# Optimization experiments

Hardware: AMD Instinct MI355X
Metric: run time of the kernel (lower is better)

## Reference

```python
import jax, jax.numpy as jnp
import numpy as np

B, L, U, H = 16, 1024, 512, 2  # batch, seq_len, units, highway_num


def setup_inputs() -> dict:
    key = jax.random.key(0)
    ks = jax.random.split(key, 8)
    s = 0.02  # weight init scale
    return {
        "inputs": jax.random.normal(ks[0], (B, L, U), dtype=jnp.float32),
        "tW": jax.random.normal(ks[1], (H, U, U), dtype=jnp.float32) * s,
        "tb": jnp.zeros((H, U), dtype=jnp.float32),
        "cW": jax.random.normal(ks[2], (H, U, U), dtype=jnp.float32) * s,
        "cb": jnp.zeros((H, U), dtype=jnp.float32),
        "aW": jax.random.normal(ks[3], (3 * U,), dtype=jnp.float32) * s,
        "ab": jnp.zeros((1,), dtype=jnp.float32),
        "frW": jax.random.normal(ks[4], (2 * U, U), dtype=jnp.float32) * s,
        "frb": jnp.zeros((U,), dtype=jnp.float32),
        "ffW": jax.random.normal(ks[5], (2 * U, U), dtype=jnp.float32) * s,
        "ffb": jnp.zeros((U,), dtype=jnp.float32),
    }


def reference(inputs, tW, tb, cW, cb, aW, ab, frW, frb, ffW, ffb):
    # Highway stack (inference: dropout is identity)
    x = inputs
    for i in range(tW.shape[0]):
        t = jax.nn.relu(x @ tW[i] + tb[i])
        c = jax.nn.sigmoid(x @ cW[i] + cb[i])
        x = t * c + x * (1.0 - c)

    # Pairwise MLP self-attention.
    # Original: A_ij = relu(dense1(concat([x_i, x_j, x_i*x_j]))).
    # Split aW = [w1; w2; w3] so we never materialize the [B,L,L,3U] tensor:
    # A_ij = relu(x_i.w1 + x_j.w2 + sum_d x_i_d * x_j_d * w3_d + b)
    u = x.shape[-1]
    w1, w2, w3 = aW[:u], aW[u:2 * u], aW[2 * u:]
    s1 = x @ w1                                    # [B,L]
    s2 = x @ w2                                    # [B,L]
    s3 = jnp.einsum('bid,bjd->bij', x * w3, x)     # [B,L,L]
    A = jax.nn.relu(s1[:, :, None] + s2[:, None, :] + s3 + ab[0])
    att = jnp.einsum('bij,bjd->bid', jax.nn.softmax(A, axis=-1), x)

    # Fuse gate. NOTE: original code uses fuse_f_dense (sigmoid) for BOTH
    # z and f (fuse_z_dense is never called), so z == f at inference.
    concat = jnp.concatenate([inputs, att], axis=-1)  # [B,L,2U]
    z = jax.nn.sigmoid(concat @ ffW + ffb)
    r = jax.nn.sigmoid(concat @ frW + frb)
    f = z
    return r * inputs + f * z
```

## Files before the change

### kernel.cpp

```cpp
#include <hip/hip_runtime.h>
#include <math.h>

typedef __bf16 bf16;
typedef __attribute__((ext_vector_type(8))) __bf16 bf16x8;
typedef __attribute__((ext_vector_type(4))) float f32x4;

#define CDIV(a,b) (((a)+(b)-1)/(b))


__device__ __forceinline__ void load_lds16(const bf16* g, bf16* l) {
  __builtin_amdgcn_global_load_lds(
      (const __attribute__((address_space(1))) unsigned int*)(g),
      (__attribute__((address_space(3))) unsigned int*)(l), 16, 0, 0);
}

struct GemmArgs {
  const bf16* A; const bf16* B; bf16* C;
  int K, lda, ldb, ldc;
  long long Ab, Bb, Cb;
  const float* s1; const float* s2; const float* abp;
  float* lsum;
  int L;
  int gxsh, gysh;
};

template<int EPI>
__global__ __launch_bounds__(256, 4)
void gemm_nt(GemmArgs g) {
  __shared__ bf16 As[128 * 64];
  __shared__ bf16 Bs[128 * 64];
  const int tid = threadIdx.x;
  const int bid = blockIdx.x;
  const int xcd = bid & 7;
  const int t = bid >> 3;
  const int bx = t & ((1 << g.gxsh) - 1);
  const int r  = t >> g.gxsh;
  const int Rx = gridDim.x >> (3 + g.gxsh);
  const int gr = xcd * Rx + r;
  const int by = gr & ((1 << g.gysh) - 1);
  const int bz = gr >> g.gysh;

  const bf16* Ag = g.A + (long long)bz * g.Ab + (long long)(by * 128) * g.lda;
  const bf16* Bg = g.B + (long long)bz * g.Bb + (long long)(bx * 128) * g.ldb;
  const int wid = tid >> 6, lane = tid & 63;
  const int wm = (wid >> 1) << 6;
  const int wn = (wid & 1) << 6;
  const int lr = lane & 15, lq = lane >> 4;

  f32x4 acc[4][4];
#pragma unroll
  for (int i = 0; i < 4; i++)
#pragma unroll
    for (int j = 0; j < 4; j++) acc[i][j] = f32x4{0.f, 0.f, 0.f, 0.f};

  const int srow8 = (tid >> 3) & 7;
  const int skc   = (tid & 7) ^ srow8;
  const int lswz  = (lr & 7);

  for (int k0 = 0; k0 < g.K; k0 += 64) {
    __syncthreads();
#pragma unroll
    for (int j = 0; j < 4; j++) {
      const int ci = (tid >> 6) * 4 + j;
      const int row = ci * 8 + srow8;
      load_lds16(Ag + (long long)row * g.lda + k0 + skc * 8, As + ci * 512);
      load_lds16(Bg + (long long)row * g.ldb + k0 + skc * 8, Bs + ci * 512);
    }
    __syncthreads();
#pragma unroll
    for (int ks = 0; ks < 2; ks++) {
      bf16x8 af[4], bfr[4];
      const int kx = (ks * 4 + lq) ^ lswz;
#pragma unroll
      for (int i = 0; i < 4; i++)
        af[i] = *(const bf16x8*)(&As[(wm + i * 16 + lr) * 64 + kx * 8]);
#pragma unroll
      for (int j = 0; j < 4; j++)
        bfr[j] = *(const bf16x8*)(&Bs[(wn + j * 16 + lr) * 64 + kx * 8]);
#pragma unroll
      for (int i = 0; i < 4; i++)
#pragma unroll
        for (int j = 0; j < 4; j++)
          acc[i][j] = __builtin_amdgcn_mfma_f32_16x16x32_bf16(af[i], bfr[j], acc[i][j], 0, 0, 0);
    }
  }

  bf16* Cg = g.C + (long long)bz * g.Cb;
#pragma unroll
  for (int i = 0; i < 4; i++) {
#pragma unroll
    for (int v = 0; v < 4; v++) {
      int row = by * 128 + wm + i * 16 + lq * 4 + v;
      float srow = 0.f;
      if (EPI == 1) srow = g.s1[bz * g.L + row] + g.abp[0];
      if (EPI == 4) srow = 1.f / g.s1[bz * g.L + row];
      float psum = 0.f;
#pragma unroll
      for (int j = 0; j < 4; j++) {
        int col = bx * 128 + wn + j * 16 + lr;
        float val = acc[i][j][v];
        if (EPI == 1) {
          val += srow + g.s2[bz * g.L + col];
          val = fminf(fmaxf(val, 0.f), 60.f);
          val = __expf(val);
          bf16 eb = (bf16)val;
          psum += (float)eb;
          Cg[(long long)row * g.ldc + col] = eb;
        } else {
          val *= srow;
          Cg[(long long)row * g.ldc + col] = (bf16)val;
        }
      }
      if (EPI == 1) {
        psum += __shfl_xor(psum, 1, 64);
        psum += __shfl_xor(psum, 2, 64);
        psum += __shfl_xor(psum, 4, 64);
        psum += __shfl_xor(psum, 8, 64);
        if (lr == 0) atomicAdd(&g.lsum[bz * g.L + row], psum);
      }
    }
  }
}

struct DualArgs {
  const bf16* A; const bf16* A2;
  const bf16* Bt;
  void* C; const void* xres;
  const float* bias_t; const float* bias_c;
  int K, ldb;
  const float* aW;
  float* s1a; float* s2a;
  bf16* q;
};

template<int EPI>
__global__ __launch_bounds__(256, 4)
void gemm_dual(DualArgs g) {
  __shared__ bf16 As[128 * 64];
  __shared__ bf16 Bs[128 * 64];
  const int tid = threadIdx.x;
  const int bid = blockIdx.x;
  const int xcd = bid & 7;
  const int t = bid >> 3;
  const int bx = t & 7;
  const int r  = t >> 3;
  const int Rx = gridDim.x >> 6;
  const int by = xcd * Rx + r;

  const int wid = tid >> 6, lane = tid & 63;
  const int wm = (wid >> 1) << 6;
  const int wn = (wid & 1) << 6;
  const int lr = lane & 15, lq = lane >> 4;

  f32x4 acc[4][4];
#pragma unroll
  for (int i = 0; i < 4; i++)
#pragma unroll
    for (int j = 0; j < 4; j++) acc[i][j] = f32x4{0.f, 0.f, 0.f, 0.f};

  const int srow8 = (tid >> 3) & 7;
  const int skc   = (tid & 7) ^ srow8;
  const int lswz  = (lr & 7);
  const long long abase = (long long)(by * 128) * 512;

  for (int k0 = 0; k0 < g.K; k0 += 64) {
    const bf16* Ak = (k0 < 512) ? g.A : g.A2;
    const int kk = k0 & 511;
    __syncthreads();
#pragma unroll
    for (int j = 0; j < 4; j++) {
      const int ci = (tid >> 6) * 4 + j;
      const int bn = ci * 8 + srow8;
      load_lds16(Ak + abase + (long long)bn * 512 + kk + skc * 8, As + ci * 512);
      const int grp = bn >> 5, r5 = bn & 31;
      const int grow = ((grp & 1) << 9) + bx * 64 + ((grp >> 1) << 5) + r5;
      load_lds16(g.Bt + (long long)grow * g.ldb + k0 + skc * 8, Bs + ci * 512);
    }
    __syncthreads();
#pragma unroll
    for (int ks = 0; ks < 2; ks++) {
      bf16x8 af[4], bfr[4];
      const int kx = (ks * 4 + lq) ^ lswz;
#pragma unroll
      for (int i = 0; i < 4; i++)
        af[i] = *(const bf16x8*)(&As[(wm + i * 16 + lr) * 64 + kx * 8]);
#pragma unroll
      for (int j = 0; j < 4; j++)
        bfr[j] = *(const bf16x8*)(&Bs[(wn + j * 16 + lr) * 64 + kx * 8]);
#pragma unroll
      for (int i = 0; i < 4; i++)
#pragma unroll
        for (int j = 0; j < 4; j++)
          acc[i][j] = __builtin_amdgcn_mfma_f32_16x16x32_bf16(af[i], bfr[j], acc[i][j], 0, 0, 0);
    }
  }

  const int colb = bx * 64 + (wn >> 1);
#pragma unroll
  for (int i = 0; i < 4; i++) {
#pragma unroll
    for (int v = 0; v < 4; v++) {
      int row = by * 128 + wm + i * 16 + lq * 4 + v;
      float p1s = 0.f, p2s = 0.f;
#pragma unroll
      for (int j = 0; j < 2; j++) {
        int col = colb + j * 16 + lr;
        long long idx = (long long)row * 512 + col;
        float p0 = acc[i][j][v] + g.bias_t[col];
        float p1 = acc[i][j + 2][v] + g.bias_c[col];
        if (EPI == 1) {
          float z = 1.f / (1.f + __expf(-p0));
          float rr = 1.f / (1.f + __expf(-p1));
          float x = ((const float*)g.xres)[idx];
          ((float*)g.C)[idx] = rr * x + z * z;
        } else {
          float tt = fmaxf(p0, 0.f);
          float c = 1.f / (1.f + __expf(-p1));
          float x = (float)((const bf16*)g.xres)[idx];
          bf16 xn = (bf16)(tt * c + x * (1.f - c));
          ((bf16*)g.C)[idx] = xn;
          if (EPI == 2) {
            float xf = (float)xn;
            p1s += xf * g.aW[col];
            p2s += xf * g.aW[512 + col];
            g.q[idx] = (bf16)(xf * g.aW[1024 + col]);
          }
        }
      }
      if (EPI == 2) {
        p1s += __shfl_xor(p1s, 1, 64);
        p1s += __shfl_xor(p1s, 2, 64);
        p1s += __shfl_xor(p1s, 4, 64);
        p1s += __shfl_xor(p1s, 8, 64);
        p2s += __shfl_xor(p2s, 1, 64);
        p2s += __shfl_xor(p2s, 2, 64);
        p2s += __shfl_xor(p2s, 4, 64);
        p2s += __shfl_xor(p2s, 8, 64);
        if (lr == 0) {
          atomicAdd(&g.s1a[row], p1s);
          atomicAdd(&g.s2a[row], p2s);
        }
      }
    }
  }
}

__global__ void wprep(const float* tW, const float* tb, const float* cW, const float* cb,
                      const float* frW, const float* frb, const float* ffW, const float* ffb,
                      bf16* w1T, bf16* w2T, float* bias1, float* bias2) {
  int idx = blockIdx.x * 256 + threadIdx.x;
  const int N1 = 1048576, N2 = 1048576;
  if (idx < N1) {
    int l = idx >> 19;
    int rem = idx & 524287;
    int n = rem >> 9, k = rem & 511;
    float v = (n < 512) ? tW[l * 262144 + k * 512 + n]
                        : cW[l * 262144 + k * 512 + (n - 512)];
    w1T[idx] = (bf16)v;
  } else if (idx < N1 + N2) {
    int j = idx - N1;
    int n = j >> 10, k = j & 1023;
    float v = (n < 512) ? ffW[k * 512 + n] : frW[k * 512 + (n - 512)];
    w2T[j] = (bf16)v;
  } else if (idx < N1 + N2 + 3072) {
    int j = idx - (N1 + N2);
    if (j < 2048) {
      int l = j >> 10, n = j & 1023;
      bias1[j] = (n < 512) ? tb[l * 512 + n] : cb[l * 512 + (n - 512)];
    } else {
      int n = j - 2048;
      bias2[n] = (n < 512) ? ffb[n] : frb[n - 512];
    }
  }
}

__global__ void init_conv(const float* inp, bf16* xb0) {
  long long i8 = ((long long)blockIdx.x * 256 + threadIdx.x) * 8;
  bf16x8 o;
#pragma unroll
  for (int k = 0; k < 8; k++) o[k] = (bf16)inp[i8 + k];
  *(bf16x8*)(xb0 + i8) = o;
}

__global__ __launch_bounds__(256) void transpose_k(const bf16* xb, bf16* xT) {
  __shared__ bf16 t[64][65];
  int b = blockIdx.z;
  int d0 = blockIdx.x * 64, j0 = blockIdx.y * 64;
  const bf16* src = xb + (long long)b * 524288;
  bf16* dst = xT + (long long)b * 524288;
  int tid = threadIdx.x;
  int rr = tid >> 3, cc = (tid & 7) * 8;
#pragma unroll
  for (int it = 0; it < 2; ++it) {
    int r = rr + it * 32;
    bf16x8 v = *(const bf16x8*)(src + (long long)(j0 + r) * 512 + d0 + cc);
#pragma unroll
    for (int k = 0; k < 8; k++) t[cc + k][r] = v[k];
  }
  __syncthreads();
#pragma unroll
  for (int it = 0; it < 2; ++it) {
    int r = rr + it * 32;
    bf16x8 v;
#pragma unroll
    for (int k = 0; k < 8; k++) v[k] = t[r][cc + k];
    *(bf16x8*)(dst + (long long)(d0 + r) * 1024 + j0 + cc) = v;
  }
}

extern "C" void kernel_launch(void* const* d_in, const int* in_sizes, int n_in,
                              void* d_out, int out_size, void* d_ws, size_t ws_size,
                              hipStream_t stream) {
  const float* inp = (const float*)d_in[0];
  const float* tW  = (const float*)d_in[1];
  const float* tb  = (const float*)d_in[2];
  const float* cW  = (const float*)d_in[3];
  const float* cb  = (const float*)d_in[4];
  const float* aW  = (const float*)d_in[5];
  const float* ab  = (const float*)d_in[6];
  const float* frW = (const float*)d_in[7];
  const float* frb = (const float*)d_in[8];
  const float* ffW = (const float*)d_in[9];
  const float* ffb = (const float*)d_in[10];
  float* out = (float*)d_out;

  char* p = (char*)d_ws;
  auto alloc = [&](size_t bytes) { char* r = p; p += (bytes + 255) & ~size_t(255); return r; };
  bf16* xb0   = (bf16*) alloc(16777216);
  bf16* x1    = (bf16*) alloc(16777216);
  bf16* x2    = (bf16*) alloc(16777216);
  bf16* q16   = (bf16*) alloc(16777216);
  bf16* xT16  = (bf16*) alloc(16777216);
  bf16* att16 = (bf16*) alloc(16777216);
  bf16* E16   = (bf16*) alloc(33554432);
  float* sred = (float*)alloc(196608);
  bf16* w1T   = (bf16*) alloc(2097152);
  bf16* w2T   = (bf16*) alloc(2097152);
  float* bias1= (float*)alloc(8192);
  float* bias2= (float*)alloc(4096);
  float* s1 = sred, *s2 = sred + 16384, *lsum = sred + 32768;

  hipMemsetAsync(sred, 0, 196608, stream);
  wprep<<<CDIV(1048576 + 1048576 + 3072, 256), 256, 0, stream>>>(
      tW, tb, cW, cb, frW, frb, ffW, ffb, w1T, w2T, bias1, bias2);
  init_conv<<<4096, 256, 0, stream>>>(inp, xb0);

  {
    DualArgs g{};
    g.A = xb0; g.A2 = xb0; g.Bt = w1T;
    g.C = x1; g.xres = xb0;
    g.bias_t = bias1; g.bias_c = bias1 + 512;
    g.K = 512; g.ldb = 512;
    gemm_dual<0><<<1024, 256, 0, stream>>>(g);
  }
  {
    DualArgs g{};
    g.A = x1; g.A2 = x1; g.Bt = w1T + 524288;
    g.C = x2; g.xres = x1;
    g.bias_t = bias1 + 1024; g.bias_c = bias1 + 1536;
    g.K = 512; g.ldb = 512;
    g.aW = aW; g.s1a = s1; g.s2a = s2; g.q = q16;
    gemm_dual<2><<<1024, 256, 0, stream>>>(g);
  }

  transpose_k<<<dim3(8, 16, 16), 256, 0, stream>>>(x2, xT16);

  {
    GemmArgs g{};
    g.A = q16; g.B = x2; g.C = E16;
    g.K = 512; g.lda = 512; g.ldb = 512; g.ldc = 1024;
    g.Ab = 524288; g.Bb = 524288; g.Cb = 1048576;
    g.s1 = s1; g.s2 = s2; g.abp = ab; g.lsum = lsum; g.L = 1024;
    g.gxsh = 3; g.gysh = 3;
    gemm_nt<1><<<1024, 256, 0, stream>>>(g);
  }
  {
    GemmArgs g{};
    g.A = E16; g.B = xT16; g.C = att16;
    g.K = 1024; g.lda = 1024; g.ldb = 1024; g.ldc = 512;
    g.Ab = 1048576; g.Bb = 524288; g.Cb = 524288;
    g.s1 = lsum; g.L = 1024;
    g.gxsh = 2; g.gysh = 3;
    gemm_nt<4><<<512, 256, 0, stream>>>(g);
  }
  {
    DualArgs g{};
    g.A = xb0; g.A2 = att16; g.Bt = w2T;
    g.C = out; g.xres = inp;
    g.bias_t = bias2; g.bias_c = bias2 + 512;
    g.K = 1024; g.ldb = 1024;
    gemm_dual<1><<<1024, 256, 0, stream>>>(g);
  }
}
```

Measured before the change: 271.7 us.

## Fuse transpose into highway GEMM epilogue and merge prep kernels

```diff
diff --git a/kernel.cpp b/kernel.cpp
--- a/kernel.cpp
+++ b/kernel.cpp
@@ -131,13 +131,15 @@
   const float* aW;
   float* s1a; float* s2a;
   bf16* q;
+  bf16* xT;
 };
 
 template<int EPI>
 __global__ __launch_bounds__(256, 4)
 void gemm_dual(DualArgs g) {
-  __shared__ bf16 As[128 * 64];
-  __shared__ bf16 Bs[128 * 64];
+  __shared__ bf16 smem[2 * 128 * 64];
+  bf16* As = smem;
+  bf16* Bs = smem + 8192;
   const int tid = threadIdx.x;
   const int bid = blockIdx.x;
   const int xcd = bid & 7;
@@ -196,6 +198,7 @@
   }
 
   const int colb = bx * 64 + (wn >> 1);
+  bf16 xn_arr[4][4][2];
 #pragma unroll
   for (int i = 0; i < 4; i++) {
 #pragma unroll
@@ -220,6 +223,7 @@
           bf16 xn = (bf16)(tt * c + x * (1.f - c));
           ((bf16*)g.C)[idx] = xn;
           if (EPI == 2) {
+            xn_arr[i][v][j] = xn;
             float xf = (float)xn;
             p1s += xf * g.aW[col];
             p2s += xf * g.aW[512 + col];
@@ -243,27 +247,59 @@
       }
     }
   }
+
+  if (EPI == 2) {
+    bf16* Ts = smem;
+    __syncthreads();
+#pragma unroll
+    for (int i = 0; i < 4; i++)
+#pragma unroll
+      for (int v = 0; v < 4; v++)
+#pragma unroll
+        for (int j = 0; j < 2; j++) {
+          int rloc = wm + i * 16 + lq * 4 + v;
+          int cloc = (wn >> 1) + j * 16 + lr;
+          Ts[cloc * 136 + rloc] = xn_arr[i][v][j];
+        }
+    __syncthreads();
+    const int b = by >> 3;
+    bf16* dst = g.xT + (long long)b * 524288 + ((by & 7) * 128);
+#pragma unroll
+    for (int it = 0; it < 2; it++) {
+      int d = (tid >> 3) + it * 32;
+      int jb = (tid & 7) * 16;
+      bf16x8 v0 = *(const bf16x8*)(&Ts[d * 136 + jb]);
+      bf16x8 v1 = *(const bf16x8*)(&Ts[d * 136 + jb + 8]);
+      long long o = (long long)(bx * 64 + d) * 1024 + jb;
+      *(bf16x8*)(dst + o) = v0;
+      *(bf16x8*)(dst + o + 8) = v1;
+    }
+  }
 }
 
-__global__ void wprep(const float* tW, const float* tb, const float* cW, const float* cb,
-                      const float* frW, const float* frb, const float* ffW, const float* ffb,
-                      bf16* w1T, bf16* w2T, float* bias1, float* bias2) {
-  int idx = blockIdx.x * 256 + threadIdx.x;
-  const int N1 = 1048576, N2 = 1048576;
+__global__ void prep(const float* tW, const float* tb, const float* cW, const float* cb,
+                     const float* frW, const float* frb, const float* ffW, const float* ffb,
+                     const float* inp, bf16* xb0,
+                     bf16* w1T, bf16* w2T, float* bias1, float* bias2, float* sred) {
+  const long long idx = (long long)blockIdx.x * 256 + threadIdx.x;
+  const long long N1 = 1048576, N2 = 1048576;
+  const long long T0 = N1 + N2 + 3072;
+  const long long T1 = T0 + 1048576;
+  const long long T2 = T1 + 12288;
   if (idx < N1) {
-    int l = idx >> 19;
-    int rem = idx & 524287;
+    int l = (int)(idx >> 19);
+    int rem = (int)(idx & 524287);
     int n = rem >> 9, k = rem & 511;
     float v = (n < 512) ? tW[l * 262144 + k * 512 + n]
                         : cW[l * 262144 + k * 512 + (n - 512)];
     w1T[idx] = (bf16)v;
   } else if (idx < N1 + N2) {
-    int j = idx - N1;
+    int j = (int)(idx - N1);
     int n = j >> 10, k = j & 1023;
     float v = (n < 512) ? ffW[k * 512 + n] : frW[k * 512 + (n - 512)];
     w2T[j] = (bf16)v;
-  } else if (idx < N1 + N2 + 3072) {
-    int j = idx - (N1 + N2);
+  } else if (idx < T0) {
+    int j = (int)(idx - (N1 + N2));
     if (j < 2048) {
       int l = j >> 10, n = j & 1023;
       bias1[j] = (n < 512) ? tb[l * 512 + n] : cb[l * 512 + (n - 512)];
@@ -271,40 +307,15 @@
       int n = j - 2048;
       bias2[n] = (n < 512) ? ffb[n] : frb[n - 512];
     }
-  }
-}
-
-__global__ void init_conv(const float* inp, bf16* xb0) {
-  long long i8 = ((long long)blockIdx.x * 256 + threadIdx.x) * 8;
-  bf16x8 o;
-#pragma unroll
-  for (int k = 0; k < 8; k++) o[k] = (bf16)inp[i8 + k];
-  *(bf16x8*)(xb0 + i8) = o;
-}
-
-__global__ __launch_bounds__(256) void transpose_k(const bf16* xb, bf16* xT) {
-  __shared__ bf16 t[64][65];
-  int b = blockIdx.z;
-  int d0 = blockIdx.x * 64, j0 = blockIdx.y * 64;
-  const bf16* src = xb + (long long)b * 524288;
-  bf16* dst = xT + (long long)b * 524288;
-  int tid = threadIdx.x;
-  int rr = tid >> 3, cc = (tid & 7) * 8;
-#pragma unroll
-  for (int it = 0; it < 2; ++it) {
-    int r = rr + it * 32;
-    bf16x8 v = *(const bf16x8*)(src + (long long)(j0 + r) * 512 + d0 + cc);
-#pragma unroll
-    for (int k = 0; k < 8; k++) t[cc + k][r] = v[k];
-  }
-  __syncthreads();
-#pragma unroll
-  for (int it = 0; it < 2; ++it) {
-    int r = rr + it * 32;
-    bf16x8 v;
-#pragma unroll
-    for (int k = 0; k < 8; k++) v[k] = t[r][cc + k];
-    *(bf16x8*)(dst + (long long)(d0 + r) * 1024 + j0 + cc) = v;
+  } else if (idx < T1) {
+    long long i8 = (idx - T0) * 8;
+    bf16x8 o;
+#pragma unroll
+    for (int k = 0; k < 8; k++) o[k] = (bf16)inp[i8 + k];
+    *(bf16x8*)(xb0 + i8) = o;
+  } else if (idx < T2) {
+    long long z = (idx - T1) * 4;
+    *(f32x4*)(sred + z) = f32x4{0.f, 0.f, 0.f, 0.f};
   }
 }
 
@@ -340,10 +351,8 @@
   float* bias2= (float*)alloc(4096);
   float* s1 = sred, *s2 = sred + 16384, *lsum = sred + 32768;
 
-  hipMemsetAsync(sred, 0, 196608, stream);
-  wprep<<<CDIV(1048576 + 1048576 + 3072, 256), 256, 0, stream>>>(
-      tW, tb, cW, cb, frW, frb, ffW, ffb, w1T, w2T, bias1, bias2);
-  init_conv<<<4096, 256, 0, stream>>>(inp, xb0);
+  prep<<<CDIV(1048576 + 1048576 + 3072 + 1048576 + 12288, 256), 256, 0, stream>>>(
+      tW, tb, cW, cb, frW, frb, ffW, ffb, inp, xb0, w1T, w2T, bias1, bias2, sred);
 
   {
     DualArgs g{};
@@ -359,12 +368,9 @@
     g.C = x2; g.xres = x1;
     g.bias_t = bias1 + 1024; g.bias_c = bias1 + 1536;
     g.K = 512; g.ldb = 512;
-    g.aW = aW; g.s1a = s1; g.s2a = s2; g.q = q16;
+    g.aW = aW; g.s1a = s1; g.s2a = s2; g.q = q16; g.xT = xT16;
     gemm_dual<2><<<1024, 256, 0, stream>>>(g);
   }
-
-  transpose_k<<<dim3(8, 16, 16), 256, 0, stream>>>(x2, xT16);
-
   {
     GemmArgs g{};
     g.A = q16; g.B = x2; g.C = E16;
```

New measurement: 277.6 us. +2.1%, slower.
